# Kernel optimization log

Hardware: AMD Instinct MI355X
Metric: run time of the kernel (lower is better)

## Reference

```python
import math
import jax, jax.numpy as jnp
import numpy as np

CT = {"SDD": 1000.0, "SCD": 500.0, "det_interval": 1.0, "num_det": 736}


def ramp_filter_np(ct, scale):
    # Standard equiangular fan-beam ramp filter (utility.ramp_filter):
    #   h[0] = 1/(8*db^2); h[n odd] = -1/(2*(pi*sin(n*db))^2); h[n even!=0] = 0
    db = ct["det_interval"] / ct["SDD"] * scale  # angular detector pitch at this scale
    n_det = int(ct["num_det"] // scale)
    n = np.arange(-(n_det - 1), n_det)  # length K = 2*n_det - 1
    h = np.zeros(n.shape, dtype=np.float32)
    h[n == 0] = 1.0 / (8.0 * db ** 2)
    odd = (n % 2) != 0
    h[odd] = -0.5 / (np.pi * np.sin(n[odd] * db)) ** 2
    return h


def setup_inputs() -> dict:
    key = jax.random.key(0)
    scale = 1
    batch, ch, view, det = 16, 1, 1152, CT["num_det"] // scale
    sinogram = jax.random.normal(key, (batch, ch, view, det), dtype=jnp.float32)
    delta_b = CT["det_interval"] / CT["SDD"]
    # recon_filter = ramp_filter * scale * delta_b, shaped [1,1,1,K] (OIHW)
    filt = ramp_filter_np(CT, scale) * scale * delta_b
    recon_filter = jnp.asarray(filt, dtype=jnp.float32)[None, None, None, :]
    return {"sinogram": sinogram, "recon_filter": recon_filter, "scale": scale}


def reference(sinogram, recon_filter, scale):
    det = sinogram.shape[-1]
    # cosine fan-beam pre-weighting
    s_range = (CT["det_interval"]
               * jnp.linspace((1.0 - det) / 2.0, (det - 1.0) / 2.0, det, dtype=jnp.float32)
               * scale) / CT["SDD"]
    cos_weight = (CT["SCD"] / 10000.0) * jnp.cos(s_range)  # [det]
    x = sinogram * cos_weight[None, None, None, :]
    # 1D ramp-filter convolution along detector axis (F.conv2d with 1xK kernel)
    K = recon_filter.shape[-1]
    pad = K // 2
    out = jax.lax.conv_general_dilated(
        x, recon_filter,
        window_strides=(1, 1),
        padding=[(0, 0), (pad, pad)],
        dimension_numbers=("NCHW", "OIHW", "NCHW"),
    )
    return out
```

## Files before the change

kernel.cpp:

```cpp
#include <hip/hip_runtime.h>

typedef unsigned short ushort_t;
typedef ushort_t u16x4 __attribute__((ext_vector_type(4)));
typedef ushort_t u16x8 __attribute__((ext_vector_type(8)));
typedef __bf16 bf16x8 __attribute__((ext_vector_type(8)));
typedef float f32x4 __attribute__((ext_vector_type(4)));

#define DET 736
#define HALF 368
#define NTT 12
#define CPB2 (NTT * 64)
#define RB 64
#define LDR 392
#define APAR (RB * LDR)


__global__ void prep_bf(const float* __restrict__ filt,
                        ushort_t* __restrict__ Be, ushort_t* __restrict__ Bo) {
    int c = blockIdx.x * blockDim.x + threadIdx.x;
    int cb  = c / CPB2;
    int rem = c - cb * CPB2;
    int t = rem >> 6, lane = rem & 63;
    int i = cb * 16 + (lane & 15);
    int quad = lane >> 4;
    u16x8 ve, vo;
#pragma unroll
    for (int e = 0; e < 8; ++e) {
        int j = t * 32 + quad * 8 + e;
        bool real = (j < HALF) && (i < HALF);
        int de = 2 * (j - i) + 1 + 735;
        int do_ = de - 2;
        de  = de  < 0 ? 0 : (de  > 1470 ? 1470 : de);
        do_ = do_ < 0 ? 0 : (do_ > 1470 ? 1470 : do_);
        float ge = 0.05f * cosf(((float)(2 * j + 1) - 367.5f) * 0.001f);
        float go = 0.05f * cosf(((float)(2 * j)     - 367.5f) * 0.001f);
        float fe = filt[de] * ge;
        float fo = filt[do_] * go;
        ve[e] = real ? __builtin_bit_cast(ushort_t, (__bf16)fe) : (ushort_t)0;
        vo[e] = real ? __builtin_bit_cast(ushort_t, (__bf16)fo) : (ushort_t)0;
    }
    *(u16x8*)(Be + (size_t)c * 8) = ve;
    *(u16x8*)(Bo + (size_t)c * 8) = vo;
}

__global__ __launch_bounds__(1024, 4) void gemm_fused(
    const float* __restrict__ sino,
    const ushort_t* __restrict__ Be, const ushort_t* __restrict__ Bo,
    const float* __restrict__ filt,
    float* __restrict__ C)
{
    __shared__ ushort_t As[2 * APAR];

    const int tid  = threadIdx.x;
    const int lane = tid & 63;
    const int wid  = tid >> 6;
    const int quad = lane >> 4;
    const int l16  = lane & 15;

    const size_t row_a0 = (size_t)blockIdx.x * RB;

    for (int c = tid; c < RB * 92; c += 1024) {
        int row = c / 92;
        int cp  = c - row * 92;
        const float* g = sino + (row_a0 + row) * DET + cp * 8;
        f32x4 lo = *(const f32x4*)g;
        f32x4 hi = *(const f32x4*)(g + 4);
        u16x4 vod, vev;
        vod[0] = __builtin_bit_cast(ushort_t, (__bf16)lo[1]);
        vod[1] = __builtin_bit_cast(ushort_t, (__bf16)lo[3]);
        vod[2] = __builtin_bit_cast(ushort_t, (__bf16)hi[1]);
        vod[3] = __builtin_bit_cast(ushort_t, (__bf16)hi[3]);
        vev[0] = __builtin_bit_cast(ushort_t, (__bf16)lo[0]);
        vev[1] = __builtin_bit_cast(ushort_t, (__bf16)lo[2]);
        vev[2] = __builtin_bit_cast(ushort_t, (__bf16)hi[0]);
        vev[3] = __builtin_bit_cast(ushort_t, (__bf16)hi[2]);
        *(u16x4*)(As + row * LDR + cp * 4)        = vod;
        *(u16x4*)(As + APAR + row * LDR + cp * 4) = vev;
    }
    if (tid < 128) {
        int p = tid & 1, row = tid >> 1;
        ushort_t* z = As + p * APAR + row * LDR + HALF;
        *(u16x8*)(z)     = (u16x8){0,0,0,0,0,0,0,0};
        *(u16x8*)(z + 8) = (u16x8){0,0,0,0,0,0,0,0};
    }
    __syncthreads();

    const int p    = wid >> 3;
    const int cb0  = (wid & 7) * 3;
    const ushort_t* Bfp = p ? Bo : Be;

    f32x4 acc[4][3];
#pragma unroll
    for (int i = 0; i < 4; ++i)
#pragma unroll
        for (int j = 0; j < 3; ++j)
            acc[i][j] = (f32x4){0.f, 0.f, 0.f, 0.f};

    int aoff[4];
#pragma unroll
    for (int mi = 0; mi < 4; ++mi)
        aoff[mi] = p * APAR + (mi * 16 + l16) * LDR + quad * 8;

    const ushort_t* pB[3];
#pragma unroll
    for (int ni = 0; ni < 3; ++ni)
        pB[ni] = Bfp + ((size_t)(cb0 + ni) * CPB2 + lane) * 8;

    u16x8 bcur[3];
#pragma unroll
    for (int ni = 0; ni < 3; ++ni)
        bcur[ni] = *(const u16x8*)(pB[ni]);

    for (int t = 0; t < NTT; ++t) {
        u16x8 bnx[3];
        if (t + 1 < NTT) {
#pragma unroll
            for (int ni = 0; ni < 3; ++ni)
                bnx[ni] = *(const u16x8*)(pB[ni] + (t + 1) * 512);
        }
        u16x8 a[4];
#pragma unroll
        for (int mi = 0; mi < 4; ++mi)
            a[mi] = *(const u16x8*)(As + aoff[mi] + t * 32);
#pragma unroll
        for (int mi = 0; mi < 4; ++mi)
#pragma unroll
            for (int ni = 0; ni < 3; ++ni)
                acc[mi][ni] = __builtin_amdgcn_mfma_f32_16x16x32_bf16(
                    __builtin_bit_cast(bf16x8, a[mi]),
                    __builtin_bit_cast(bf16x8, bcur[ni]),
                    acc[mi][ni], 0, 0, 0);
        if (t + 1 < NTT) {
#pragma unroll
            for (int ni = 0; ni < 3; ++ni) bcur[ni] = bnx[ni];
        }
    }

    const float h0 = filt[735];
#pragma unroll
    for (int ni = 0; ni < 3; ++ni) {
        int ic   = (cb0 + ni) * 16 + l16;
        int colg = 2 * ic + p;
        if (colg < DET) {
            float gw = h0 * 0.05f * cosf(((float)colg - 367.5f) * 0.001f);
#pragma unroll
            for (int mi = 0; mi < 4; ++mi) {
#pragma unroll
                for (int r = 0; r < 4; ++r) {
                    size_t rowg = row_a0 + mi * 16 + quad * 4 + r;
                    float xd = sino[rowg * DET + colg];
                    C[rowg * DET + colg] = acc[mi][ni][r] + gw * xd;
                }
            }
        }
    }
}

extern "C" void kernel_launch(void* const* d_in, const int* in_sizes, int n_in,
                              void* d_out, int out_size, void* d_ws, size_t ws_size,
                              hipStream_t stream) {
    const float* sino = (const float*)d_in[0];
    const float* filt = (const float*)d_in[1];
    (void)in_sizes; (void)n_in; (void)out_size; (void)ws_size;

    const size_t BSZ = (size_t)24 * CPB2 * 8;

    ushort_t* Be = (ushort_t*)d_ws;
    ushort_t* Bo = Be + BSZ;
    float* out = (float*)d_out;

    prep_bf<<<72, 256, 0, stream>>>(filt, Be, Bo);

    gemm_fused<<<dim3(288), 1024, 0, stream>>>(sino, Be, Bo, filt, out);
}
```

Before: 153.0 us.

## Keep sinogram rows in registers per wave and drop shared-memory staging

```diff
diff --git a/kernel.cpp b/kernel.cpp
--- a/kernel.cpp
+++ b/kernel.cpp
@@ -1,7 +1,6 @@
 #include <hip/hip_runtime.h>
 
 typedef unsigned short ushort_t;
-typedef ushort_t u16x4 __attribute__((ext_vector_type(4)));
 typedef ushort_t u16x8 __attribute__((ext_vector_type(8)));
 typedef __bf16 bf16x8 __attribute__((ext_vector_type(8)));
 typedef float f32x4 __attribute__((ext_vector_type(4)));
@@ -10,9 +9,12 @@
 #define HALF 368
 #define NTT 12
 #define CPB2 (NTT * 64)
-#define RB 64
-#define LDR 392
-#define APAR (RB * LDR)
+#define NRB 1152
+#define NCB 23
+
+__device__ __forceinline__ ushort_t f2bf(float f) {
+    return __builtin_bit_cast(ushort_t, (__bf16)f);
+}
 
 
 __global__ void prep_bf(const float* __restrict__ filt,
@@ -36,122 +38,94 @@
         float go = 0.05f * cosf(((float)(2 * j)     - 367.5f) * 0.001f);
         float fe = filt[de] * ge;
         float fo = filt[do_] * go;
-        ve[e] = real ? __builtin_bit_cast(ushort_t, (__bf16)fe) : (ushort_t)0;
-        vo[e] = real ? __builtin_bit_cast(ushort_t, (__bf16)fo) : (ushort_t)0;
+        ve[e] = real ? f2bf(fe) : (ushort_t)0;
+        vo[e] = real ? f2bf(fo) : (ushort_t)0;
     }
     *(u16x8*)(Be + (size_t)c * 8) = ve;
     *(u16x8*)(Bo + (size_t)c * 8) = vo;
 }
 
-__global__ __launch_bounds__(1024, 4) void gemm_fused(
+__global__ __launch_bounds__(256) void gemm_direct(
     const float* __restrict__ sino,
     const ushort_t* __restrict__ Be, const ushort_t* __restrict__ Bo,
     const float* __restrict__ filt,
     float* __restrict__ C)
 {
-    __shared__ ushort_t As[2 * APAR];
-
     const int tid  = threadIdx.x;
     const int lane = tid & 63;
     const int wid  = tid >> 6;
     const int quad = lane >> 4;
     const int l16  = lane & 15;
 
-    const size_t row_a0 = (size_t)blockIdx.x * RB;
+    const int rblk = blockIdx.x * 4 + wid;
 
-    for (int c = tid; c < RB * 92; c += 1024) {
-        int row = c / 92;
-        int cp  = c - row * 92;
-        const float* g = sino + (row_a0 + row) * DET + cp * 8;
-        f32x4 lo = *(const f32x4*)g;
-        f32x4 hi = *(const f32x4*)(g + 4);
-        u16x4 vod, vev;
-        vod[0] = __builtin_bit_cast(ushort_t, (__bf16)lo[1]);
-        vod[1] = __builtin_bit_cast(ushort_t, (__bf16)lo[3]);
-        vod[2] = __builtin_bit_cast(ushort_t, (__bf16)hi[1]);
-        vod[3] = __builtin_bit_cast(ushort_t, (__bf16)hi[3]);
-        vev[0] = __builtin_bit_cast(ushort_t, (__bf16)lo[0]);
-        vev[1] = __builtin_bit_cast(ushort_t, (__bf16)lo[2]);
-        vev[2] = __builtin_bit_cast(ushort_t, (__bf16)hi[0]);
-        vev[3] = __builtin_bit_cast(ushort_t, (__bf16)hi[2]);
-        *(u16x4*)(As + row * LDR + cp * 4)        = vod;
-        *(u16x4*)(As + APAR + row * LDR + cp * 4) = vev;
-    }
-    if (tid < 128) {
-        int p = tid & 1, row = tid >> 1;
-        ushort_t* z = As + p * APAR + row * LDR + HALF;
-        *(u16x8*)(z)     = (u16x8){0,0,0,0,0,0,0,0};
-        *(u16x8*)(z + 8) = (u16x8){0,0,0,0,0,0,0,0};
-    }
-    __syncthreads();
-
-    const int p    = wid >> 3;
-    const int cb0  = (wid & 7) * 3;
-    const ushort_t* Bfp = p ? Bo : Be;
-
-    f32x4 acc[4][3];
+    const float* arow = sino + ((size_t)rblk * 16 + l16) * DET;
+    u16x8 ae[NTT], ao[NTT];
 #pragma unroll
-    for (int i = 0; i < 4; ++i)
-#pragma unroll
-        for (int j = 0; j < 3; ++j)
-            acc[i][j] = (f32x4){0.f, 0.f, 0.f, 0.f};
-
-    int aoff[4];
-#pragma unroll
-    for (int mi = 0; mi < 4; ++mi)
-        aoff[mi] = p * APAR + (mi * 16 + l16) * LDR + quad * 8;
-
-    const ushort_t* pB[3];
-#pragma unroll
-    for (int ni = 0; ni < 3; ++ni)
-        pB[ni] = Bfp + ((size_t)(cb0 + ni) * CPB2 + lane) * 8;
-
-    u16x8 bcur[3];
-#pragma unroll
-    for (int ni = 0; ni < 3; ++ni)
-        bcur[ni] = *(const u16x8*)(pB[ni]);
-
     for (int t = 0; t < NTT; ++t) {
-        u16x8 bnx[3];
-        if (t + 1 < NTT) {
-#pragma unroll
-            for (int ni = 0; ni < 3; ++ni)
-                bnx[ni] = *(const u16x8*)(pB[ni] + (t + 1) * 512);
-        }
-        u16x8 a[4];
-#pragma unroll
-        for (int mi = 0; mi < 4; ++mi)
-            a[mi] = *(const u16x8*)(As + aoff[mi] + t * 32);
-#pragma unroll
-        for (int mi = 0; mi < 4; ++mi)
-#pragma unroll
-            for (int ni = 0; ni < 3; ++ni)
-                acc[mi][ni] = __builtin_amdgcn_mfma_f32_16x16x32_bf16(
-                    __builtin_bit_cast(bf16x8, a[mi]),
-                    __builtin_bit_cast(bf16x8, bcur[ni]),
-                    acc[mi][ni], 0, 0, 0);
-        if (t + 1 < NTT) {
-#pragma unroll
-            for (int ni = 0; ni < 3; ++ni) bcur[ni] = bnx[ni];
+        const int j0 = t * 32 + quad * 8;
+        if (j0 < HALF) {
+            const float* g = arow + 2 * j0;
+            f32x4 w0 = *(const f32x4*)(g);
+            f32x4 w1 = *(const f32x4*)(g + 4);
+            f32x4 w2 = *(const f32x4*)(g + 8);
+            f32x4 w3 = *(const f32x4*)(g + 12);
+            u16x8 ve, vo;
+            ve[0] = f2bf(w0[1]); vo[0] = f2bf(w0[0]);
+            ve[1] = f2bf(w0[3]); vo[1] = f2bf(w0[2]);
+            ve[2] = f2bf(w1[1]); vo[2] = f2bf(w1[0]);
+            ve[3] = f2bf(w1[3]); vo[3] = f2bf(w1[2]);
+            ve[4] = f2bf(w2[1]); vo[4] = f2bf(w2[0]);
+            ve[5] = f2bf(w2[3]); vo[5] = f2bf(w2[2]);
+            ve[6] = f2bf(w3[1]); vo[6] = f2bf(w3[0]);
+            ve[7] = f2bf(w3[3]); vo[7] = f2bf(w3[2]);
+            ae[t] = ve; ao[t] = vo;
+        } else {
+            ae[t] = (u16x8){0,0,0,0,0,0,0,0};
+            ao[t] = (u16x8){0,0,0,0,0,0,0,0};
         }
     }
 
     const float h0 = filt[735];
+    const size_t lane_off = (size_t)lane * 8;
+
+#pragma unroll 1
+    for (int cb = 0; cb < NCB; ++cb) {
+        const ushort_t* be_p = Be + (size_t)cb * (CPB2 * 8) + lane_off;
+        const ushort_t* bo_p = Bo + (size_t)cb * (CPB2 * 8) + lane_off;
+
+        f32x4 acc_e = (f32x4){0.f, 0.f, 0.f, 0.f};
+        f32x4 acc_o = (f32x4){0.f, 0.f, 0.f, 0.f};
+
+        u16x8 be_c = *(const u16x8*)(be_p);
+        u16x8 bo_c = *(const u16x8*)(bo_p);
 #pragma unroll
-    for (int ni = 0; ni < 3; ++ni) {
-        int ic   = (cb0 + ni) * 16 + l16;
-        int colg = 2 * ic + p;
-        if (colg < DET) {
-            float gw = h0 * 0.05f * cosf(((float)colg - 367.5f) * 0.001f);
+        for (int t = 0; t < NTT; ++t) {
+            u16x8 be_n, bo_n;
+            if (t + 1 < NTT) {
+                be_n = *(const u16x8*)(be_p + (t + 1) * 512);
+                bo_n = *(const u16x8*)(bo_p + (t + 1) * 512);
+            }
+            acc_e = __builtin_amdgcn_mfma_f32_16x16x32_bf16(
+                __builtin_bit_cast(bf16x8, ae[t]),
+                __builtin_bit_cast(bf16x8, be_c), acc_e, 0, 0, 0);
+            acc_o = __builtin_amdgcn_mfma_f32_16x16x32_bf16(
+                __builtin_bit_cast(bf16x8, ao[t]),
+                __builtin_bit_cast(bf16x8, bo_c), acc_o, 0, 0, 0);
+            if (t + 1 < NTT) { be_c = be_n; bo_c = bo_n; }
+        }
+
+        const int ic = cb * 16 + l16;
+        const float gw_e = h0 * 0.05f * cosf(((float)(2 * ic)     - 367.5f) * 0.001f);
+        const float gw_o = h0 * 0.05f * cosf(((float)(2 * ic + 1) - 367.5f) * 0.001f);
 #pragma unroll
-            for (int mi = 0; mi < 4; ++mi) {
-#pragma unroll
-                for (int r = 0; r < 4; ++r) {
-                    size_t rowg = row_a0 + mi * 16 + quad * 4 + r;
-                    float xd = sino[rowg * DET + colg];
-                    C[rowg * DET + colg] = acc[mi][ni][r] + gw * xd;
-                }
-            }
+        for (int r = 0; r < 4; ++r) {
+            const size_t rowg = (size_t)rblk * 16 + quad * 4 + r;
+            const float2 xd = *(const float2*)(sino + rowg * DET + 2 * ic);
+            float2 o;
+            o.x = acc_e[r] + gw_e * xd.x;
+            o.y = acc_o[r] + gw_o * xd.y;
+            *(float2*)(C + rowg * DET + 2 * ic) = o;
         }
     }
 }
@@ -171,5 +145,5 @@
 
     prep_bf<<<72, 256, 0, stream>>>(filt, Be, Bo);
 
-    gemm_fused<<<dim3(288), 1024, 0, stream>>>(sino, Be, Bo, filt, out);
+    gemm_direct<<<NRB / 4, 256, 0, stream>>>(sino, Be, Bo, filt, out);
 }
```

After: 158.3 us. +3.5%, slower.
